# Optimization experiments

Measured on AMD Instinct MI355X. Metric: run time of the kernel, lower is better.

The kernel has to match this reference:

```python
import jax, jax.numpy as jnp
import numpy as np

N_BATTERS = 5000
N_PITCHERS = 2000
N_PAIRS = 10_000_000


def setup_inputs() -> dict:
    key = jax.random.key(0)
    k1, k2, k3, k4, k5, k6, k7 = jax.random.split(key, 7)
    v1 = jax.random.normal(k1, (N_BATTERS,), dtype=jnp.float32)
    v2 = jax.random.normal(k2, (N_PITCHERS,), dtype=jnp.float32)
    weight = jax.random.uniform(k3, (1,), dtype=jnp.float32)
    event1 = jax.random.uniform(k4, (N_PAIRS,), dtype=jnp.float32)
    event2 = jax.random.uniform(k5, (N_PAIRS,), dtype=jnp.float32)
    batter_idx = jax.random.randint(k6, (N_PAIRS,), 0, N_BATTERS, dtype=jnp.int32)
    pitcher_idx = jax.random.randint(k7, (N_PAIRS,), 0, N_PITCHERS, dtype=jnp.int32)
    return {
        "v1": v1,
        "v2": v2,
        "weight": weight,
        "event1": event1,
        "event2": event2,
        "batter_idx": batter_idx,
        "pitcher_idx": pitcher_idx,
    }


def reference(v1, v2, weight, event1, event2, batter_idx, pitcher_idx):
    # gather per-pair player strengths
    b = v1[batter_idx]            # [N]
    p = v2[pitcher_idx]           # [N]
    w = weight[0]
    z = w * b + (1.0 - w) * p     # logit per pair
    # temp/(1+temp) with temp=exp(z) == sigmoid(z)
    prob = jax.nn.sigmoid(z)
    prob = jnp.clip(prob, 1e-06, 0.999999)
    ll = jnp.sum(event1 * jnp.log(prob) + event2 * jnp.log1p(-prob))
    return ll
```

## Files before the change

### kernel.cpp

```cpp
#include <hip/hip_runtime.h>

#define BLOCK 512
#define GRID  1024
#define NB_MAX 5000
#define NP_MAX 2000

__global__ __launch_bounds__(BLOCK, 8) void vs_ll_kernel(
    const float* __restrict__ v1, const float* __restrict__ v2,
    const float* __restrict__ weight,
    const float* __restrict__ e1, const float* __restrict__ e2,
    const int*  __restrict__ bidx, const int* __restrict__ pidx,
    int nb, int np, int n, float* __restrict__ partials)
{
    __shared__ float s_v1[NB_MAX];
    __shared__ float s_v2[NP_MAX];
    __shared__ float s_red[BLOCK / 64];

    for (int i = threadIdx.x; i < nb; i += BLOCK) s_v1[i] = v1[i];
    for (int i = threadIdx.x; i < np; i += BLOCK) s_v2[i] = v2[i];
    __syncthreads();

    const float w     = weight[0];
    const float onemw = 1.0f - w;
    const float LOG_LO = -13.815511f;
    const float LOG_HI = -1.0000005e-6f;

    float acc = 0.0f;

    const int n4     = n >> 2;
    const int gid    = blockIdx.x * BLOCK + threadIdx.x;
    const int stride = GRID * BLOCK;
    const float4* e1v = (const float4*)e1;
    const float4* e2v = (const float4*)e2;
    const int4*   bv  = (const int4*)bidx;
    const int4*   pv  = (const int4*)pidx;

    int  i     = gid;
    bool valid = (i < n4);
    float4 a, c; int4 b, p;
    if (valid) { a = e1v[i]; c = e2v[i]; b = bv[i]; p = pv[i]; }

    while (valid) {
        const int  inext = i + stride;
        const bool vnext = (inext < n4);
        float4 a2, c2; int4 b2, p2;
        if (vnext) { a2 = e1v[inext]; c2 = e2v[inext]; b2 = bv[inext]; p2 = pv[inext]; }

        float bb[4] = { s_v1[b.x], s_v1[b.y], s_v1[b.z], s_v1[b.w] };
        float pp[4] = { s_v2[p.x], s_v2[p.y], s_v2[p.z], s_v2[p.w] };
        float u1[4] = { a.x, a.y, a.z, a.w };
        float u2[4] = { c.x, c.y, c.z, c.w };

        #pragma unroll
        for (int j = 0; j < 4; ++j) {
            float z  = fmaf(w, bb[j], onemw * pp[j]);
            float az = fabsf(z);
            float l  = __logf(1.0f + __expf(-az));
            float logp = -(fmaxf(-z, 0.0f) + l);
            float logq = -(fmaxf( z, 0.0f) + l);
            logp = fminf(fmaxf(logp, LOG_LO), LOG_HI);
            logq = fminf(fmaxf(logq, LOG_LO), LOG_HI);
            acc = fmaf(u1[j], logp, acc);
            acc = fmaf(u2[j], logq, acc);
        }

        a = a2; c = c2; b = b2; p = p2;
        i = inext; valid = vnext;
    }

    for (int t = (n4 << 2) + gid; t < n; t += stride) {
        float z  = fmaf(w, s_v1[bidx[t]], onemw * s_v2[pidx[t]]);
        float az = fabsf(z);
        float l  = __logf(1.0f + __expf(-az));
        float logp = fminf(fmaxf(-(fmaxf(-z, 0.0f) + l), LOG_LO), LOG_HI);
        float logq = fminf(fmaxf(-(fmaxf( z, 0.0f) + l), LOG_LO), LOG_HI);
        acc = fmaf(e1[t], logp, acc);
        acc = fmaf(e2[t], logq, acc);
    }

    #pragma unroll
    for (int off = 32; off > 0; off >>= 1)
        acc += __shfl_down(acc, off, 64);

    const int lane = threadIdx.x & 63;
    const int wid  = threadIdx.x >> 6;
    if (lane == 0) s_red[wid] = acc;
    __syncthreads();
    if (threadIdx.x == 0) {
        float t = 0.0f;
        #pragma unroll
        for (int k = 0; k < BLOCK / 64; ++k) t += s_red[k];
        partials[blockIdx.x] = t;
    }
}

__global__ __launch_bounds__(256) void vs_reduce_kernel(
    const float* __restrict__ partials, int nparts, float* __restrict__ out)
{
    __shared__ float s_red[4];
    float acc = 0.0f;
    for (int i = threadIdx.x; i < nparts; i += 256) acc += partials[i];
    #pragma unroll
    for (int off = 32; off > 0; off >>= 1)
        acc += __shfl_down(acc, off, 64);
    const int lane = threadIdx.x & 63;
    const int wid  = threadIdx.x >> 6;
    if (lane == 0) s_red[wid] = acc;
    __syncthreads();
    if (threadIdx.x == 0) {
        float t = 0.0f;
        #pragma unroll
        for (int k = 0; k < 4; ++k) t += s_red[k];
        out[0] = t;
    }
}

extern "C" void kernel_launch(void* const* d_in, const int* in_sizes, int n_in,
                              void* d_out, int out_size, void* d_ws, size_t ws_size,
                              hipStream_t stream) {
    const float* v1     = (const float*)d_in[0];
    const float* v2     = (const float*)d_in[1];
    const float* weight = (const float*)d_in[2];
    const float* e1     = (const float*)d_in[3];
    const float* e2     = (const float*)d_in[4];
    const int*   bidx   = (const int*)d_in[5];
    const int*   pidx   = (const int*)d_in[6];

    const int nb = in_sizes[0];
    const int np = in_sizes[1];
    const int n  = in_sizes[3];

    float* partials = (float*)d_ws;
    float* out      = (float*)d_out;

    vs_ll_kernel<<<GRID, BLOCK, 0, stream>>>(v1, v2, weight, e1, e2, bidx, pidx,
                                             nb, np, n, partials);
    vs_reduce_kernel<<<1, 256, 0, stream>>>(partials, GRID, out);
}
```

Measured before the change: 34.19 us.

## Batch five vector loads per thread with masked clamped indices, halve block size

The main loop switches from single-step software prefetch to a five-way unrolled batch. Each thread issues all 20 vector loads up front, using clamped indices and a multiplicative mask instead of branches, then computes on them. This is meant to put more memory requests in flight per thread. The block drops to 256 threads with four blocks per CU, which halves the total thread count and changes how often each block refills its shared-memory tables. The shared-memory table fill now uses float4 copies. The trade-off is more registers and redundant masked loads on the last partial iteration.

```diff
diff --git a/kernel.cpp b/kernel.cpp
--- a/kernel.cpp
+++ b/kernel.cpp
@@ -1,11 +1,12 @@
 #include <hip/hip_runtime.h>
 
-#define BLOCK 512
+#define BLOCK 256
 #define GRID  1024
+#define UF    5
 #define NB_MAX 5000
 #define NP_MAX 2000
 
-__global__ __launch_bounds__(BLOCK, 8) void vs_ll_kernel(
+__global__ __launch_bounds__(BLOCK, 4) void vs_ll_kernel(
     const float* __restrict__ v1, const float* __restrict__ v2,
     const float* __restrict__ weight,
     const float* __restrict__ e1, const float* __restrict__ e2,
@@ -16,8 +17,17 @@
     __shared__ float s_v2[NP_MAX];
     __shared__ float s_red[BLOCK / 64];
 
-    for (int i = threadIdx.x; i < nb; i += BLOCK) s_v1[i] = v1[i];
-    for (int i = threadIdx.x; i < np; i += BLOCK) s_v2[i] = v2[i];
+    {
+        const float4* v1v = (const float4*)v1;
+        const float4* v2v = (const float4*)v2;
+        float4* s1v = (float4*)s_v1;
+        float4* s2v = (float4*)s_v2;
+        const int nb4 = nb >> 2, np4 = np >> 2;
+        for (int i = threadIdx.x; i < nb4; i += BLOCK) s1v[i] = v1v[i];
+        for (int i = threadIdx.x; i < np4; i += BLOCK) s2v[i] = v2v[i];
+        for (int i = (nb4 << 2) + threadIdx.x; i < nb; i += BLOCK) s_v1[i] = v1[i];
+        for (int i = (np4 << 2) + threadIdx.x; i < np; i += BLOCK) s_v2[i] = v2[i];
+    }
     __syncthreads();
 
     const float w     = weight[0];
@@ -27,48 +37,55 @@
 
     float acc = 0.0f;
 
-    const int n4     = n >> 2;
-    const int gid    = blockIdx.x * BLOCK + threadIdx.x;
-    const int stride = GRID * BLOCK;
+    const int n4 = n >> 2;
+    const int T  = GRID * BLOCK;
+    const int gid = blockIdx.x * BLOCK + threadIdx.x;
     const float4* e1v = (const float4*)e1;
     const float4* e2v = (const float4*)e2;
     const int4*   bv  = (const int4*)bidx;
     const int4*   pv  = (const int4*)pidx;
 
-    int  i     = gid;
-    bool valid = (i < n4);
-    float4 a, c; int4 b, p;
-    if (valid) { a = e1v[i]; c = e2v[i]; b = bv[i]; p = pv[i]; }
-
-    while (valid) {
-        const int  inext = i + stride;
-        const bool vnext = (inext < n4);
-        float4 a2, c2; int4 b2, p2;
-        if (vnext) { a2 = e1v[inext]; c2 = e2v[inext]; b2 = bv[inext]; p2 = pv[inext]; }
-
-        float bb[4] = { s_v1[b.x], s_v1[b.y], s_v1[b.z], s_v1[b.w] };
-        float pp[4] = { s_v2[p.x], s_v2[p.y], s_v2[p.z], s_v2[p.w] };
-        float u1[4] = { a.x, a.y, a.z, a.w };
-        float u2[4] = { c.x, c.y, c.z, c.w };
+    for (int base = gid; base < n4; base += UF * T) {
+        float4 A[UF], C[UF];
+        int4   B[UF], P[UF];
+        float  msk[UF];
 
         #pragma unroll
-        for (int j = 0; j < 4; ++j) {
-            float z  = fmaf(w, bb[j], onemw * pp[j]);
-            float az = fabsf(z);
-            float l  = __logf(1.0f + __expf(-az));
-            float logp = -(fmaxf(-z, 0.0f) + l);
-            float logq = -(fmaxf( z, 0.0f) + l);
-            logp = fminf(fmaxf(logp, LOG_LO), LOG_HI);
-            logq = fminf(fmaxf(logq, LOG_LO), LOG_HI);
-            acc = fmaf(u1[j], logp, acc);
-            acc = fmaf(u2[j], logq, acc);
+        for (int k = 0; k < UF; ++k) {
+            int slot = base + k * T;
+            int idx  = slot < n4 ? slot : n4 - 1;
+            msk[k] = slot < n4 ? 1.0f : 0.0f;
+            A[k] = e1v[idx];
+            C[k] = e2v[idx];
+            B[k] = bv[idx];
+            P[k] = pv[idx];
         }
 
-        a = a2; c = c2; b = b2; p = p2;
-        i = inext; valid = vnext;
+        #pragma unroll
+        for (int k = 0; k < UF; ++k) {
+            float bb[4] = { s_v1[B[k].x], s_v1[B[k].y], s_v1[B[k].z], s_v1[B[k].w] };
+            float pp[4] = { s_v2[P[k].x], s_v2[P[k].y], s_v2[P[k].z], s_v2[P[k].w] };
+            float u1[4] = { A[k].x, A[k].y, A[k].z, A[k].w };
+            float u2[4] = { C[k].x, C[k].y, C[k].z, C[k].w };
+
+            float gacc = 0.0f;
+            #pragma unroll
+            for (int j = 0; j < 4; ++j) {
+                float z  = fmaf(w, bb[j], onemw * pp[j]);
+                float az = fabsf(z);
+                float l  = __logf(1.0f + __expf(-az));
+                float logp = -(fmaxf(-z, 0.0f) + l);
+                float logq = -(fmaxf( z, 0.0f) + l);
+                logp = fminf(fmaxf(logp, LOG_LO), LOG_HI);
+                logq = fminf(fmaxf(logq, LOG_LO), LOG_HI);
+                gacc = fmaf(u1[j], logp, gacc);
+                gacc = fmaf(u2[j], logq, gacc);
+            }
+            acc = fmaf(msk[k], gacc, acc);
+        }
     }
 
-    for (int t = (n4 << 2) + gid; t < n; t += stride) {
+    for (int t = (n4 << 2) + gid; t < n; t += T) {
         float z  = fmaf(w, s_v1[bidx[t]], onemw * s_v2[pidx[t]]);
         float az = fabsf(z);
         float l  = __logf(1.0f + __expf(-az));
```

After: 38.27 us. 11.9% more time.
